# Optimization experiments

Hardware: AMD Instinct MI355X
Metric: run time of the kernel (lower is better)

The kernel has to match this reference:

```python
import jax, jax.numpy as jnp
import numpy as np

N, E, G, D, C = 50000, 800000, 512, 128, 10
BN_EPS = 1e-5

def setup_inputs() -> dict:
    key = jax.random.key(0)
    ks = jax.random.split(key, 12)
    inp = {
        'x': jnp.zeros((N,), dtype=jnp.int64 if jax.config.jax_enable_x64 else jnp.int32),
        'edge_index': jax.random.randint(ks[0], (2, E), 0, N),
        'batch_ids': jnp.sort(jax.random.randint(ks[1], (N,), 0, G)),
        'emb': jax.random.normal(ks[2], (1, D), jnp.float32),
        'W1a': jax.random.normal(ks[3], (D, D), jnp.float32) * 0.05,
        'b1a': jnp.zeros((D,), jnp.float32),
        'g1': jnp.ones((D,), jnp.float32),
        'be1': jnp.zeros((D,), jnp.float32),
        'W1b': jax.random.normal(ks[4], (D, D), jnp.float32) * 0.05,
        'b1b': jnp.zeros((D,), jnp.float32),
        'W2a': jax.random.normal(ks[5], (D, D), jnp.float32) * 0.05,
        'b2a': jnp.zeros((D,), jnp.float32),
        'g2': jnp.ones((D,), jnp.float32),
        'be2': jnp.zeros((D,), jnp.float32),
        'W2b': jax.random.normal(ks[6], (D, D), jnp.float32) * 0.05,
        'b2b': jnp.zeros((D,), jnp.float32),
        'Wm': jax.random.normal(ks[7], (D, C), jnp.float32) * 0.05,
        'bm': jnp.zeros((C,), jnp.float32),
        'Wx': jax.random.normal(ks[8], (D, C), jnp.float32) * 0.05,
        'bx': jnp.zeros((C,), jnp.float32),
        'ens_w': jnp.array([0.6, 0.4], jnp.float32),
    }
    return inp

def _gin_layer(h, src, dst, Wa, ba, g, be, Wb, bb):
    # GINConv, eps=0: mlp(x + sum_{j in N(i)} x_j)
    agg = jax.ops.segment_sum(h[src], dst, num_segments=N)  # [N, D]
    z = (h + agg) @ Wa + ba
    mu = jnp.mean(z, axis=0)
    var = jnp.var(z, axis=0)  # biased, as torch BN training forward
    z = (z - mu) * jax.lax.rsqrt(var + BN_EPS) * g + be
    z = jax.nn.relu(z)  # dropout is identity in eval
    return z @ Wb + bb

def reference(x, edge_index, batch_ids, emb, W1a, b1a, g1, be1, W1b, b1b,
              W2a, b2a, g2, be2, W2b, b2b, Wm, bm, Wx, bx, ens_w):
    src, dst = edge_index[0], edge_index[1]
    h0 = emb[x]  # [N, D] (all indices 0)
    h1 = _gin_layer(h0, src, dst, W1a, b1a, g1, be1, W1b, b1b)
    h2 = _gin_layer(h1, src, dst, W2a, b2a, g2, be2, W2b, b2b) + h1
    # global mean / max pooling over batch segments
    counts = jax.ops.segment_sum(jnp.ones((N,), h2.dtype), batch_ids, num_segments=G)
    mean_repr = jax.ops.segment_sum(h2, batch_ids, num_segments=G) / jnp.maximum(counts, 1.0)[:, None]
    max_repr = jax.ops.segment_max(h2, batch_ids, num_segments=G)
    max_repr = jnp.where(jnp.isfinite(max_repr), max_repr, 0.0)  # empty segments -> 0
    logits_mean = mean_repr @ Wm + bm
    logits_max = max_repr @ Wx + bx
    w = jax.nn.softmax(ens_w)
    ensemble_logits = w[0] * logits_mean + w[1] * logits_max
    return (ensemble_logits, logits_mean, logits_max, (mean_repr, max_repr))
```

## Files before the change

kernel.cpp:

```cpp
#include <hip/hip_runtime.h>
#include <math.h>

#define N_NODES  50000
#define N_EDGES  800000
#define N_GRAPHS 512
#define DIM      128
#define NCLS     10
#define KH       64
#define KW       32
#define KT       128
#define OVF_CAP  65536
#define BN_EPS   1e-5f

#define NB_GEMM  ((N_NODES + 63) / 64)


__global__ void k_zero(uint4* __restrict__ p, long long n4) {
    long long i = (long long)blockIdx.x * blockDim.x + threadIdx.x;
    if (i < n4) p[i] = make_uint4(0u, 0u, 0u, 0u);
}

__global__ void k_count_deg(const int* __restrict__ dst, int* __restrict__ deg) {
    int e = blockIdx.x * blockDim.x + threadIdx.x;
    if (e < N_EDGES) atomicAdd(&deg[dst[e]], 1);
}

__device__ inline int lower_bound_i(const int* __restrict__ a, int n, int v) {
    int lo = 0, hi = n;
    while (lo < hi) {
        int mid = (lo + hi) >> 1;
        if (a[mid] < v) lo = mid + 1; else hi = mid;
    }
    return lo;
}

__global__ __launch_bounds__(512) void k_prep2(
        const int* __restrict__ batch, int* __restrict__ seg,
        const int* __restrict__ deg,
        const float* __restrict__ emb, const float* __restrict__ W1a,
        const float* __restrict__ g1, const float* __restrict__ be1,
        float* __restrict__ A, float* __restrict__ B) {
    __shared__ unsigned long long sred[512];
    const int t = threadIdx.x;
    seg[t] = lower_bound_i(batch, N_NODES, t);
    if (t == 0) seg[N_GRAPHS] = N_NODES;
    unsigned long long s = 0;
    for (int i = t; i < N_NODES; i += 512) {
        unsigned long long d = (unsigned long long)(unsigned int)deg[i];
        s += d * d;
    }
    sred[t] = s;
    __syncthreads();
    for (int st = 256; st > 0; st >>= 1) {
        if (t < st) sred[t] += sred[t + st];
        __syncthreads();
    }
    if (t < DIM) {
        float u = 0.f;
        for (int k = 0; k < DIM; ++k) u += emb[k] * W1a[k * DIM + t];
        double mdeg = (double)N_EDGES / (double)N_NODES;
        double vdeg = (double)sred[0] / (double)N_NODES - mdeg * mdeg;
        float var = (float)((double)u * (double)u * vdeg);
        float rs  = rsqrtf(var + BN_EPS);
        float a   = u * rs * g1[t];
        A[t] = a;
        B[t] = be1[t] - (float)mdeg * a;
    }
}

__global__ void k_tables(const float* __restrict__ A, const float* __restrict__ B,
                         const float* __restrict__ W1b, const float* __restrict__ b1b,
                         const float* __restrict__ W2a,
                         float* __restrict__ table, float* __restrict__ table2) {
    int k = blockIdx.x, d = threadIdx.x;
    __shared__ float r[DIM];
    __shared__ float t[DIM];
    float kf = (float)k;
    r[d] = fmaxf(kf * A[d] + B[d], 0.f);
    __syncthreads();
    float acc = b1b[d];
    for (int j = 0; j < DIM; ++j) acc += r[j] * W1b[j * DIM + d];
    table[(size_t)k * DIM + d] = acc;
    t[d] = acc;
    __syncthreads();
    float acc2 = 0.f;
    for (int j = 0; j < DIM; ++j) acc2 += t[j] * W2a[j * DIM + d];
    table2[(size_t)k * DIM + d] = acc2;
}

__global__ void k_edges(const int* __restrict__ src, const int* __restrict__ dst,
                        const int* __restrict__ deg, unsigned int* __restrict__ m,
                        unsigned int* __restrict__ ovf_cnt, int* __restrict__ ovf_buf) {
    int e = blockIdx.x * blockDim.x + threadIdx.x;
    if (e >= N_EDGES) return;
    int s = src[e], dd = dst[e];
    int k = deg[s];
    if (k < KH) {
        atomicAdd(&m[(size_t)dd * KW + (k >> 1)], 1u << ((k & 1) << 4));
    } else {
        unsigned int idx = atomicAdd(ovf_cnt, 1u);
        if (idx < OVF_CAP) {
            ovf_buf[2 * idx] = dd;
            ovf_buf[2 * idx + 1] = k;
        }
    }
}

__global__ __launch_bounds__(256) void k_gemm1(
        const unsigned int* __restrict__ m, const int* __restrict__ deg,
        const float* __restrict__ table2, const float* __restrict__ b2a,
        float* __restrict__ z2, float* __restrict__ spart,
        const unsigned int* __restrict__ ovf_cnt, const int* __restrict__ ovf_buf) {
    __shared__ __align__(16) float lds_t2[64 * 128];
    __shared__ __align__(16) unsigned int lds_m[64 * 33];
    const int t = threadIdx.x;
    const int i0 = blockIdx.x * 64;
    #pragma unroll
    for (int q = 0; q < 8; ++q) {
        int idx = t + 256 * q;
        int row = idx >> 5, c = (idx & 31) << 2;
        *(float4*)&lds_t2[row * 128 + c] = *(const float4*)&table2[(size_t)row * 128 + c];
    }
    #pragma unroll
    for (int q = 0; q < 2; ++q) {
        int idx = t + 256 * q;
        int row = idx >> 3, c = (idx & 7) << 2;
        uint4 v = make_uint4(0u, 0u, 0u, 0u);
        if (i0 + row < N_NODES) v = *(const uint4*)&m[(size_t)(i0 + row) * KW + c];
        lds_m[row * 33 + c + 0] = v.x;
        lds_m[row * 33 + c + 1] = v.y;
        lds_m[row * 33 + c + 2] = v.z;
        lds_m[row * 33 + c + 3] = v.w;
    }
    __syncthreads();

    const int g = t >> 5;
    const int c4 = (t & 31) << 2;
    const int rbase = g * 8;
    float acc[8][4] = {};
    #pragma unroll 4
    for (int w = 0; w < KW; ++w) {
        float4 ta = *(const float4*)&lds_t2[(2 * w) * 128 + c4];
        float4 tb = *(const float4*)&lds_t2[(2 * w + 1) * 128 + c4];
        #pragma unroll
        for (int r = 0; r < 8; ++r) {
            unsigned int mw = lds_m[(rbase + r) * 33 + w];
            float lo = (float)(mw & 0xFFFFu);
            float hi = (float)(mw >> 16);
            acc[r][0] += lo * ta.x + hi * tb.x;
            acc[r][1] += lo * ta.y + hi * tb.y;
            acc[r][2] += lo * ta.z + hi * tb.z;
            acc[r][3] += lo * ta.w + hi * tb.w;
        }
    }

    unsigned int nov = *ovf_cnt;
    if (nov > OVF_CAP) nov = OVF_CAP;
    for (unsigned int u = 0; u < nov; ++u) {
        int dd = ovf_buf[2 * u];
        int r = dd - i0;
        if (r >= 0 && r < 64 && (r >> 3) == g) {
            int kk = ovf_buf[2 * u + 1]; if (kk > KT - 1) kk = KT - 1;
            float4 tv = *(const float4*)&table2[(size_t)kk * DIM + c4];
            acc[r & 7][0] += tv.x; acc[r & 7][1] += tv.y;
            acc[r & 7][2] += tv.z; acc[r & 7][3] += tv.w;
        }
    }

    float4 bb = *(const float4*)&b2a[c4];
    float s4[4] = {0.f, 0.f, 0.f, 0.f};
    float q4[4] = {0.f, 0.f, 0.f, 0.f};
    #pragma unroll
    for (int r = 0; r < 8; ++r) {
        int row = i0 + rbase + r;
        if (row < N_NODES) {
            int kk = deg[row];
            float4 self;
            if (kk < KH) self = *(const float4*)&lds_t2[kk * 128 + c4];
            else {
                if (kk > KT - 1) kk = KT - 1;
                self = *(const float4*)&table2[(size_t)kk * DIM + c4];
            }
            float v0 = acc[r][0] + self.x + bb.x;
            float v1 = acc[r][1] + self.y + bb.y;
            float v2 = acc[r][2] + self.z + bb.z;
            float v3 = acc[r][3] + self.w + bb.w;
            *(float4*)&z2[(size_t)row * DIM + c4] = make_float4(v0, v1, v2, v3);
            s4[0] += v0; q4[0] += v0 * v0;
            s4[1] += v1; q4[1] += v1 * v1;
            s4[2] += v2; q4[2] += v2 * v2;
            s4[3] += v3; q4[3] += v3 * v3;
        }
    }
    __syncthreads();
    float* red = (float*)lds_m;
    #pragma unroll
    for (int j = 0; j < 4; ++j) {
        red[g * 128 + c4 + j] = s4[j];
        red[1024 + g * 128 + c4 + j] = q4[j];
    }
    __syncthreads();
    if (t < 128) {
        float ss = 0.f, qq = 0.f;
        #pragma unroll
        for (int gg = 0; gg < 8; ++gg) {
            ss += red[gg * 128 + t];
            qq += red[1024 + gg * 128 + t];
        }
        spart[(size_t)blockIdx.x * 256 + t] = ss;
        spart[(size_t)blockIdx.x * 256 + 128 + t] = qq;
    }
}

__global__ __launch_bounds__(1024) void k_fin2(
        const float* __restrict__ spart,
        const float* __restrict__ g2, const float* __restrict__ be2,
        float* __restrict__ A2, float* __restrict__ B2) {
    __shared__ double red[4 * 256];
    int t = threadIdx.x & 255;
    int q = threadIdx.x >> 8;
    double acc = 0.0;
    #pragma unroll 4
    for (int b = q; b < NB_GEMM; b += 4) acc += (double)spart[(size_t)b * 256 + t];
    red[q * 256 + t] = acc;
    __syncthreads();
    if (threadIdx.x < 256)
        red[threadIdx.x] = red[threadIdx.x] + red[256 + threadIdx.x] +
                           red[512 + threadIdx.x] + red[768 + threadIdx.x];
    __syncthreads();
    if (threadIdx.x < 128) {
        double mu = red[threadIdx.x] / (double)N_NODES;
        double var = red[128 + threadIdx.x] / (double)N_NODES - mu * mu;
        float rs = rsqrtf((float)var + BN_EPS);
        float a = rs * g2[threadIdx.x];
        A2[threadIdx.x] = a;
        B2[threadIdx.x] = be2[threadIdx.x] - (float)mu * a;
    }
}

__global__ __launch_bounds__(256) void k_gemm2(
        const float* __restrict__ z2, const float* __restrict__ A2, const float* __restrict__ B2,
        const float* __restrict__ W2b, const float* __restrict__ b2b,
        const float* __restrict__ table, const int* __restrict__ deg,
        float* __restrict__ h2) {
    __shared__ __align__(16) float lds_zn[64 * 132];
    const int t = threadIdx.x;
    const int i0 = blockIdx.x * 64;
    #pragma unroll
    for (int q = 0; q < 8; ++q) {
        int idx = t + 256 * q;
        int row = idx >> 5, cc = (idx & 31) << 2;
        float4 zv = make_float4(0.f, 0.f, 0.f, 0.f);
        if (i0 + row < N_NODES) zv = *(const float4*)&z2[(size_t)(i0 + row) * DIM + cc];
        float4 av = *(const float4*)&A2[cc];
        float4 bv = *(const float4*)&B2[cc];
        lds_zn[row * 132 + cc + 0] = fmaxf(zv.x * av.x + bv.x, 0.f);
        lds_zn[row * 132 + cc + 1] = fmaxf(zv.y * av.y + bv.y, 0.f);
        lds_zn[row * 132 + cc + 2] = fmaxf(zv.z * av.z + bv.z, 0.f);
        lds_zn[row * 132 + cc + 3] = fmaxf(zv.w * av.w + bv.w, 0.f);
    }
    __syncthreads();

    const int g = t >> 5;
    const int c4 = (t & 31) << 2;
    const int rbase = g * 8;
    float acc[8][4] = {};
    #pragma unroll 2
    for (int kb = 0; kb < 32; ++kb) {
        const int k0 = kb * 4;
        float4 w0 = *(const float4*)&W2b[(size_t)(k0 + 0) * DIM + c4];
        float4 w1 = *(const float4*)&W2b[(size_t)(k0 + 1) * DIM + c4];
        float4 w2 = *(const float4*)&W2b[(size_t)(k0 + 2) * DIM + c4];
        float4 w3 = *(const float4*)&W2b[(size_t)(k0 + 3) * DIM + c4];
        #pragma unroll
        for (int r = 0; r < 8; ++r) {
            float4 zr = *(const float4*)&lds_zn[(rbase + r) * 132 + k0];
            acc[r][0] += zr.x * w0.x + zr.y * w1.x + zr.z * w2.x + zr.w * w3.x;
            acc[r][1] += zr.x * w0.y + zr.y * w1.y + zr.z * w2.y + zr.w * w3.y;
            acc[r][2] += zr.x * w0.z + zr.y * w1.z + zr.z * w2.z + zr.w * w3.z;
            acc[r][3] += zr.x * w0.w + zr.y * w1.w + zr.z * w2.w + zr.w * w3.w;
        }
    }

    float4 bbv = *(const float4*)&b2b[c4];
    #pragma unroll
    for (int r = 0; r < 8; ++r) {
        int row = i0 + rbase + r;
        if (row < N_NODES) {
            int kk = deg[row]; if (kk > KT - 1) kk = KT - 1;
            float4 tb = *(const float4*)&table[(size_t)kk * DIM + c4];
            float4 o;
            o.x = acc[r][0] + bbv.x + tb.x;
            o.y = acc[r][1] + bbv.y + tb.y;
            o.z = acc[r][2] + bbv.z + tb.z;
            o.w = acc[r][3] + bbv.w + tb.w;
            *(float4*)&h2[(size_t)row * DIM + c4] = o;
        }
    }
}

__global__ __launch_bounds__(1024) void k_poolhead(
        const float* __restrict__ h2, const int* __restrict__ seg,
        const float* __restrict__ Wm, const float* __restrict__ bm,
        const float* __restrict__ Wx, const float* __restrict__ bx,
        const float* __restrict__ ensw,
        float* __restrict__ out_ens, float* __restrict__ out_lm,
        float* __restrict__ out_lx,
        float* __restrict__ out_mean, float* __restrict__ out_max) {
    __shared__ float reds[32 * 132];
    __shared__ float redm[32 * 132];
    int g = blockIdx.x;
    int s0 = seg[g], e0 = seg[g + 1];
    int rg = threadIdx.x >> 5;
    int c4 = (threadIdx.x & 31) << 2;
    float s[4] = {0.f, 0.f, 0.f, 0.f};
    float mx[4] = {-INFINITY, -INFINITY, -INFINITY, -INFINITY};
    for (int i = s0 + rg; i < e0; i += 32) {
        float4 v = *(const float4*)&h2[(size_t)i * DIM + c4];
        s[0] += v.x; mx[0] = fmaxf(mx[0], v.x);
        s[1] += v.y; mx[1] = fmaxf(mx[1], v.y);
        s[2] += v.z; mx[2] = fmaxf(mx[2], v.z);
        s[3] += v.w; mx[3] = fmaxf(mx[3], v.w);
    }
    #pragma unroll
    for (int j = 0; j < 4; ++j) {
        reds[rg * 132 + c4 + j] = s[j];
        redm[rg * 132 + c4 + j] = mx[j];
    }
    __syncthreads();
    for (int step = 16; step >= 1; step >>= 1) {
        if (rg < step) {
            #pragma unroll
            for (int j = 0; j < 4; ++j) {
                reds[rg * 132 + c4 + j] += reds[(rg + step) * 132 + c4 + j];
                redm[rg * 132 + c4 + j] = fmaxf(redm[rg * 132 + c4 + j],
                                                redm[(rg + step) * 132 + c4 + j]);
            }
        }
        __syncthreads();
    }
    if (rg == 0) {
        int cnt = e0 - s0;
        float denom = (float)(cnt > 0 ? cnt : 1);
        #pragma unroll
        for (int j = 0; j < 4; ++j) {
            float mean = reds[c4 + j] / denom;
            float mxv  = (cnt > 0) ? redm[c4 + j] : 0.f;
            out_mean[(size_t)g * DIM + c4 + j] = mean;
            out_max[(size_t)g * DIM + c4 + j]  = mxv;
            reds[c4 + j] = mean;
            redm[c4 + j] = mxv;
        }
    }
    __syncthreads();
    int t = threadIdx.x;
    if (t < NCLS) {
        float lm = bm[t], lx = bx[t];
        for (int d = 0; d < DIM; ++d) {
            lm += reds[d] * Wm[d * NCLS + t];
            lx += redm[d] * Wx[d * NCLS + t];
        }
        float a0 = ensw[0], a1 = ensw[1];
        float mw = fmaxf(a0, a1);
        float e0v = expf(a0 - mw), e1v = expf(a1 - mw);
        float inv = 1.f / (e0v + e1v);
        out_lm[(size_t)g * NCLS + t] = lm;
        out_lx[(size_t)g * NCLS + t] = lx;
        out_ens[(size_t)g * NCLS + t] = (e0v * inv) * lm + (e1v * inv) * lx;
    }
}


extern "C" void kernel_launch(void* const* d_in, const int* in_sizes, int n_in,
                              void* d_out, int out_size, void* d_ws, size_t ws_size,
                              hipStream_t stream) {
    const int* edge = (const int*)d_in[1];
    const int* src = edge;
    const int* dst = edge + N_EDGES;
    const int* batch = (const int*)d_in[2];
    const float* emb = (const float*)d_in[3];
    const float* W1a = (const float*)d_in[4];
    const float* g1  = (const float*)d_in[6];
    const float* be1 = (const float*)d_in[7];
    const float* W1b = (const float*)d_in[8];
    const float* b1b = (const float*)d_in[9];
    const float* W2a = (const float*)d_in[10];
    const float* b2a = (const float*)d_in[11];
    const float* g2  = (const float*)d_in[12];
    const float* be2 = (const float*)d_in[13];
    const float* W2b = (const float*)d_in[14];
    const float* b2b = (const float*)d_in[15];
    const float* Wm  = (const float*)d_in[16];
    const float* bm  = (const float*)d_in[17];
    const float* Wx  = (const float*)d_in[18];
    const float* bx  = (const float*)d_in[19];
    const float* ensw = (const float*)d_in[20];

    char* ws = (char*)d_ws;
    size_t off = 0;
    auto take = [&](size_t bytes) {
        char* p = ws + off;
        off += (bytes + 511) & ~(size_t)511;
        return p;
    };
    int* deg                  = (int*)take((size_t)N_NODES * 4);
    unsigned int* m           = (unsigned int*)take((size_t)N_NODES * KW * 4);
    unsigned int* ovf_cnt     = (unsigned int*)take(4);
    size_t zbytes = off;
    float* spart              = (float*)take((size_t)NB_GEMM * 256 * 4);
    int* ovf_buf              = (int*)take((size_t)OVF_CAP * 2 * 4);
    float* table              = (float*)take((size_t)KT * DIM * 4);
    float* table2             = (float*)take((size_t)KT * DIM * 4);
    float* A                  = (float*)take(DIM * 4);
    float* B                  = (float*)take(DIM * 4);
    float* A2                 = (float*)take(DIM * 4);
    float* B2                 = (float*)take(DIM * 4);
    int* seg                  = (int*)take((size_t)(N_GRAPHS + 1) * 4);
    float* z2                 = (float*)take((size_t)N_NODES * DIM * 4);
    float* h2                 = (float*)take((size_t)N_NODES * DIM * 4);
    (void)ws_size; (void)in_sizes; (void)n_in; (void)out_size;

    float* out      = (float*)d_out;
    float* out_ens  = out;
    float* out_lm   = out + (size_t)N_GRAPHS * NCLS;
    float* out_lx   = out + 2 * (size_t)N_GRAPHS * NCLS;
    float* out_mean = out + 3 * (size_t)N_GRAPHS * NCLS;
    float* out_max  = out_mean + (size_t)N_GRAPHS * DIM;

    long long n4 = (long long)(zbytes >> 4);
    k_zero<<<(int)((n4 + 255) / 256), 256, 0, stream>>>((uint4*)ws, n4);
    k_count_deg<<<(N_EDGES + 255) / 256, 256, 0, stream>>>(dst, deg);
    k_edges<<<(N_EDGES + 255) / 256, 256, 0, stream>>>(src, dst, deg, m, ovf_cnt, ovf_buf);
    k_prep2<<<1, 512, 0, stream>>>(batch, seg, deg, emb, W1a, g1, be1, A, B);
    k_tables<<<KT, DIM, 0, stream>>>(A, B, W1b, b1b, W2a, table, table2);
    k_gemm1<<<NB_GEMM, 256, 0, stream>>>(m, deg, table2, b2a, z2, spart, ovf_cnt, ovf_buf);
    k_fin2<<<1, 1024, 0, stream>>>(spart, g2, be2, A2, B2);
    k_gemm2<<<NB_GEMM, 256, 0, stream>>>(z2, A2, B2, W2b, b2b, table, deg, h2);
    k_poolhead<<<N_GRAPHS, 1024, 0, stream>>>(h2, seg, Wm, bm, Wx, bx, ensw,
                                              out_ens, out_lm, out_lx, out_mean, out_max);
}
```

Baseline: 201.5 us.

## Recompute layer-2 pre-activations in gemm2 instead of storing z2; parallelize reductions

```diff
diff --git a/kernel.cpp b/kernel.cpp
--- a/kernel.cpp
+++ b/kernel.cpp
@@ -12,7 +12,10 @@
 #define OVF_CAP  65536
 #define BN_EPS   1e-5f
 
-#define NB_GEMM  ((N_NODES + 63) / 64)
+#define TR       32
+#define NB_GEMM  ((N_NODES + TR - 1) / TR)
+#define NB_DEG   32
+#define FIN_A    96
 
 
 __global__ void k_zero(uint4* __restrict__ p, long long n4) {
@@ -20,9 +23,15 @@
     if (i < n4) p[i] = make_uint4(0u, 0u, 0u, 0u);
 }
 
-__global__ void k_count_deg(const int* __restrict__ dst, int* __restrict__ deg) {
+__global__ void k_count_deg(const int4* __restrict__ dst4, int* __restrict__ deg) {
     int e = blockIdx.x * blockDim.x + threadIdx.x;
-    if (e < N_EDGES) atomicAdd(&deg[dst[e]], 1);
+    if (e < N_EDGES / 4) {
+        int4 d = dst4[e];
+        atomicAdd(&deg[d.x], 1);
+        atomicAdd(&deg[d.y], 1);
+        atomicAdd(&deg[d.z], 1);
+        atomicAdd(&deg[d.w], 1);
+    }
 }
 
 __device__ inline int lower_bound_i(const int* __restrict__ a, int n, int v) {
@@ -34,49 +43,51 @@
     return lo;
 }
 
-__global__ __launch_bounds__(512) void k_prep2(
-        const int* __restrict__ batch, int* __restrict__ seg,
-        const int* __restrict__ deg,
-        const float* __restrict__ emb, const float* __restrict__ W1a,
-        const float* __restrict__ g1, const float* __restrict__ be1,
-        float* __restrict__ A, float* __restrict__ B) {
-    __shared__ unsigned long long sred[512];
+__global__ __launch_bounds__(1024) void k_sumdeg2(
+        const int* __restrict__ deg, unsigned long long* __restrict__ dpart,
+        const int* __restrict__ batch, int* __restrict__ seg) {
+    __shared__ unsigned long long lds[1024];
     const int t = threadIdx.x;
-    seg[t] = lower_bound_i(batch, N_NODES, t);
-    if (t == 0) seg[N_GRAPHS] = N_NODES;
+    if (blockIdx.x == 0) {
+        if (t < N_GRAPHS) seg[t] = lower_bound_i(batch, N_NODES, t);
+        if (t == 0) seg[N_GRAPHS] = N_NODES;
+    }
     unsigned long long s = 0;
-    for (int i = t; i < N_NODES; i += 512) {
+    for (int i = blockIdx.x * 1024 + t; i < N_NODES; i += NB_DEG * 1024) {
         unsigned long long d = (unsigned long long)(unsigned int)deg[i];
         s += d * d;
     }
-    sred[t] = s;
-    __syncthreads();
-    for (int st = 256; st > 0; st >>= 1) {
-        if (t < st) sred[t] += sred[t + st];
+    lds[t] = s;
+    __syncthreads();
+    for (int st = 512; st > 0; st >>= 1) {
+        if (t < st) lds[t] += lds[t + st];
         __syncthreads();
     }
-    if (t < DIM) {
-        float u = 0.f;
-        for (int k = 0; k < DIM; ++k) u += emb[k] * W1a[k * DIM + t];
-        double mdeg = (double)N_EDGES / (double)N_NODES;
-        double vdeg = (double)sred[0] / (double)N_NODES - mdeg * mdeg;
-        float var = (float)((double)u * (double)u * vdeg);
-        float rs  = rsqrtf(var + BN_EPS);
-        float a   = u * rs * g1[t];
-        A[t] = a;
-        B[t] = be1[t] - (float)mdeg * a;
-    }
-}
-
-__global__ void k_tables(const float* __restrict__ A, const float* __restrict__ B,
+    if (t == 0) dpart[blockIdx.x] = lds[0];
+}
+
+__global__ void k_tables(const unsigned long long* __restrict__ dpart,
+                         const float* __restrict__ emb, const float* __restrict__ W1a,
+                         const float* __restrict__ g1, const float* __restrict__ be1,
                          const float* __restrict__ W1b, const float* __restrict__ b1b,
                          const float* __restrict__ W2a,
                          float* __restrict__ table, float* __restrict__ table2) {
     int k = blockIdx.x, d = threadIdx.x;
     __shared__ float r[DIM];
     __shared__ float t[DIM];
+    float u = 0.f;
+    for (int j = 0; j < DIM; ++j) u += emb[j] * W1a[j * DIM + d];
+    unsigned long long s2 = 0;
+    #pragma unroll 8
+    for (int b = 0; b < NB_DEG; ++b) s2 += dpart[b];
+    double mdeg = (double)N_EDGES / (double)N_NODES;
+    double vdeg = (double)s2 / (double)N_NODES - mdeg * mdeg;
+    float var = (float)((double)u * (double)u * vdeg);
+    float rs  = rsqrtf(var + BN_EPS);
+    float A   = u * rs * g1[d];
+    float B   = be1[d] - (float)mdeg * A;
     float kf = (float)k;
-    r[d] = fmaxf(kf * A[d] + B[d], 0.f);
+    r[d] = fmaxf(kf * A + B, 0.f);
     __syncthreads();
     float acc = b1b[d];
     for (int j = 0; j < DIM; ++j) acc += r[j] * W1b[j * DIM + d];
@@ -88,43 +99,41 @@
     table2[(size_t)k * DIM + d] = acc2;
 }
 
-__global__ void k_edges(const int* __restrict__ src, const int* __restrict__ dst,
+__global__ void k_edges(const int4* __restrict__ src4, const int4* __restrict__ dst4,
                         const int* __restrict__ deg, unsigned int* __restrict__ m,
                         unsigned int* __restrict__ ovf_cnt, int* __restrict__ ovf_buf) {
     int e = blockIdx.x * blockDim.x + threadIdx.x;
-    if (e >= N_EDGES) return;
-    int s = src[e], dd = dst[e];
-    int k = deg[s];
-    if (k < KH) {
-        atomicAdd(&m[(size_t)dd * KW + (k >> 1)], 1u << ((k & 1) << 4));
-    } else {
-        unsigned int idx = atomicAdd(ovf_cnt, 1u);
-        if (idx < OVF_CAP) {
-            ovf_buf[2 * idx] = dd;
-            ovf_buf[2 * idx + 1] = k;
-        }
-    }
-}
-
-__global__ __launch_bounds__(256) void k_gemm1(
+    if (e >= N_EDGES / 4) return;
+    int4 sv = src4[e];
+    int4 dv = dst4[e];
+    int ss[4] = {sv.x, sv.y, sv.z, sv.w};
+    int dd[4] = {dv.x, dv.y, dv.z, dv.w};
+    #pragma unroll
+    for (int j = 0; j < 4; ++j) {
+        int k = deg[ss[j]];
+        if (k < KH) {
+            atomicAdd(&m[(size_t)dd[j] * KW + (k >> 1)], 1u << ((k & 1) << 4));
+        } else {
+            unsigned int idx = atomicAdd(ovf_cnt, 1u);
+            if (idx < OVF_CAP) {
+                ovf_buf[2 * idx] = dd[j];
+                ovf_buf[2 * idx + 1] = k;
+            }
+        }
+    }
+}
+
+__global__ __launch_bounds__(256) void k_gemm1s(
         const unsigned int* __restrict__ m, const int* __restrict__ deg,
         const float* __restrict__ table2, const float* __restrict__ b2a,
-        float* __restrict__ z2, float* __restrict__ spart,
+        float* __restrict__ spart,
         const unsigned int* __restrict__ ovf_cnt, const int* __restrict__ ovf_buf) {
-    __shared__ __align__(16) float lds_t2[64 * 128];
-    __shared__ __align__(16) unsigned int lds_m[64 * 33];
+    __shared__ __align__(16) unsigned int lds_m[TR * 33];
+    __shared__ float red[2048];
     const int t = threadIdx.x;
-    const int i0 = blockIdx.x * 64;
-    #pragma unroll
-    for (int q = 0; q < 8; ++q) {
-        int idx = t + 256 * q;
-        int row = idx >> 5, c = (idx & 31) << 2;
-        *(float4*)&lds_t2[row * 128 + c] = *(const float4*)&table2[(size_t)row * 128 + c];
-    }
-    #pragma unroll
-    for (int q = 0; q < 2; ++q) {
-        int idx = t + 256 * q;
-        int row = idx >> 3, c = (idx & 7) << 2;
+    const int i0 = blockIdx.x * TR;
+    {
+        int row = t >> 3, c = (t & 7) << 2;
         uint4 v = make_uint4(0u, 0u, 0u, 0u);
         if (i0 + row < N_NODES) v = *(const uint4*)&m[(size_t)(i0 + row) * KW + c];
         lds_m[row * 33 + c + 0] = v.x;
@@ -136,14 +145,14 @@
 
     const int g = t >> 5;
     const int c4 = (t & 31) << 2;
-    const int rbase = g * 8;
-    float acc[8][4] = {};
+    const int rbase = g * 4;
+    float acc[4][4] = {};
     #pragma unroll 4
     for (int w = 0; w < KW; ++w) {
-        float4 ta = *(const float4*)&lds_t2[(2 * w) * 128 + c4];
-        float4 tb = *(const float4*)&lds_t2[(2 * w + 1) * 128 + c4];
+        float4 ta = *(const float4*)&table2[(size_t)(2 * w) * DIM + c4];
+        float4 tb = *(const float4*)&table2[(size_t)(2 * w + 1) * DIM + c4];
         #pragma unroll
-        for (int r = 0; r < 8; ++r) {
+        for (int r = 0; r < 4; ++r) {
             unsigned int mw = lds_m[(rbase + r) * 33 + w];
             float lo = (float)(mw & 0xFFFFu);
             float hi = (float)(mw >> 16);
@@ -153,17 +162,16 @@
             acc[r][3] += lo * ta.w + hi * tb.w;
         }
     }
-
     unsigned int nov = *ovf_cnt;
     if (nov > OVF_CAP) nov = OVF_CAP;
     for (unsigned int u = 0; u < nov; ++u) {
         int dd = ovf_buf[2 * u];
         int r = dd - i0;
-        if (r >= 0 && r < 64 && (r >> 3) == g) {
+        if (r >= 0 && r < TR && (r >> 2) == g) {
             int kk = ovf_buf[2 * u + 1]; if (kk > KT - 1) kk = KT - 1;
             float4 tv = *(const float4*)&table2[(size_t)kk * DIM + c4];
-            acc[r & 7][0] += tv.x; acc[r & 7][1] += tv.y;
-            acc[r & 7][2] += tv.z; acc[r & 7][3] += tv.w;
+            acc[r & 3][0] += tv.x; acc[r & 3][1] += tv.y;
+            acc[r & 3][2] += tv.z; acc[r & 3][3] += tv.w;
         }
     }
 
@@ -171,29 +179,21 @@
     float s4[4] = {0.f, 0.f, 0.f, 0.f};
     float q4[4] = {0.f, 0.f, 0.f, 0.f};
     #pragma unroll
-    for (int r = 0; r < 8; ++r) {
+    for (int r = 0; r < 4; ++r) {
         int row = i0 + rbase + r;
         if (row < N_NODES) {
-            int kk = deg[row];
-            float4 self;
-            if (kk < KH) self = *(const float4*)&lds_t2[kk * 128 + c4];
-            else {
-                if (kk > KT - 1) kk = KT - 1;
-                self = *(const float4*)&table2[(size_t)kk * DIM + c4];
-            }
+            int kk = deg[row]; if (kk > KT - 1) kk = KT - 1;
+            float4 self = *(const float4*)&table2[(size_t)kk * DIM + c4];
             float v0 = acc[r][0] + self.x + bb.x;
             float v1 = acc[r][1] + self.y + bb.y;
             float v2 = acc[r][2] + self.z + bb.z;
             float v3 = acc[r][3] + self.w + bb.w;
-            *(float4*)&z2[(size_t)row * DIM + c4] = make_float4(v0, v1, v2, v3);
             s4[0] += v0; q4[0] += v0 * v0;
             s4[1] += v1; q4[1] += v1 * v1;
             s4[2] += v2; q4[2] += v2 * v2;
             s4[3] += v3; q4[3] += v3 * v3;
         }
     }
-    __syncthreads();
-    float* red = (float*)lds_m;
     #pragma unroll
     for (int j = 0; j < 4; ++j) {
         red[g * 128 + c4 + j] = s4[j];
@@ -212,59 +212,116 @@
     }
 }
 
-__global__ __launch_bounds__(1024) void k_fin2(
-        const float* __restrict__ spart,
+__global__ __launch_bounds__(256) void k_fin2a(
+        const float* __restrict__ spart, double* __restrict__ spart2) {
+    const int t = threadIdx.x;
+    double s = 0.0;
+    for (int r = blockIdx.x; r < NB_GEMM; r += FIN_A)
+        s += (double)spart[(size_t)r * 256 + t];
+    spart2[(size_t)blockIdx.x * 256 + t] = s;
+}
+
+__global__ __launch_bounds__(256) void k_fin2b(
+        const double* __restrict__ spart2,
         const float* __restrict__ g2, const float* __restrict__ be2,
         float* __restrict__ A2, float* __restrict__ B2) {
-    __shared__ double red[4 * 256];
-    int t = threadIdx.x & 255;
-    int q = threadIdx.x >> 8;
-    double acc = 0.0;
-    #pragma unroll 4
-    for (int b = q; b < NB_GEMM; b += 4) acc += (double)spart[(size_t)b * 256 + t];
-    red[q * 256 + t] = acc;
-    __syncthreads();
-    if (threadIdx.x < 256)
-        red[threadIdx.x] = red[threadIdx.x] + red[256 + threadIdx.x] +
-                           red[512 + threadIdx.x] + red[768 + threadIdx.x];
-    __syncthreads();
-    if (threadIdx.x < 128) {
-        double mu = red[threadIdx.x] / (double)N_NODES;
-        double var = red[128 + threadIdx.x] / (double)N_NODES - mu * mu;
+    __shared__ double red[256];
+    const int t = threadIdx.x;
+    double s = 0.0;
+    #pragma unroll 8
+    for (int b = 0; b < FIN_A; ++b) s += spart2[(size_t)b * 256 + t];
+    red[t] = s;
+    __syncthreads();
+    if (t < 128) {
+        double mu = red[t] / (double)N_NODES;
+        double var = red[128 + t] / (double)N_NODES - mu * mu;
         float rs = rsqrtf((float)var + BN_EPS);
-        float a = rs * g2[threadIdx.x];
-        A2[threadIdx.x] = a;
-        B2[threadIdx.x] = be2[threadIdx.x] - (float)mu * a;
+        float a = rs * g2[t];
+        A2[t] = a;
+        B2[t] = be2[t] - (float)mu * a;
     }
 }
 
 __global__ __launch_bounds__(256) void k_gemm2(
-        const float* __restrict__ z2, const float* __restrict__ A2, const float* __restrict__ B2,
+        const unsigned int* __restrict__ m, const int* __restrict__ deg,
+        const float* __restrict__ table2, const float* __restrict__ b2a,
+        const float* __restrict__ A2, const float* __restrict__ B2,
         const float* __restrict__ W2b, const float* __restrict__ b2b,
-        const float* __restrict__ table, const int* __restrict__ deg,
-        float* __restrict__ h2) {
-    __shared__ __align__(16) float lds_zn[64 * 132];
+        const float* __restrict__ table, float* __restrict__ h2,
+        const unsigned int* __restrict__ ovf_cnt, const int* __restrict__ ovf_buf) {
+    __shared__ __align__(16) unsigned int lds_m[TR * 33];
+    __shared__ __align__(16) float lds_zn[TR * 132];
     const int t = threadIdx.x;
-    const int i0 = blockIdx.x * 64;
-    #pragma unroll
-    for (int q = 0; q < 8; ++q) {
-        int idx = t + 256 * q;
-        int row = idx >> 5, cc = (idx & 31) << 2;
-        float4 zv = make_float4(0.f, 0.f, 0.f, 0.f);
-        if (i0 + row < N_NODES) zv = *(const float4*)&z2[(size_t)(i0 + row) * DIM + cc];
-        float4 av = *(const float4*)&A2[cc];
-        float4 bv = *(const float4*)&B2[cc];
-        lds_zn[row * 132 + cc + 0] = fmaxf(zv.x * av.x + bv.x, 0.f);
-        lds_zn[row * 132 + cc + 1] = fmaxf(zv.y * av.y + bv.y, 0.f);
-        lds_zn[row * 132 + cc + 2] = fmaxf(zv.z * av.z + bv.z, 0.f);
-        lds_zn[row * 132 + cc + 3] = fmaxf(zv.w * av.w + bv.w, 0.f);
+    const int i0 = blockIdx.x * TR;
+    {
+        int row = t >> 3, c = (t & 7) << 2;
+        uint4 v = make_uint4(0u, 0u, 0u, 0u);
+        if (i0 + row < N_NODES) v = *(const uint4*)&m[(size_t)(i0 + row) * KW + c];
+        lds_m[row * 33 + c + 0] = v.x;
+        lds_m[row * 33 + c + 1] = v.y;
+        lds_m[row * 33 + c + 2] = v.z;
+        lds_m[row * 33 + c + 3] = v.w;
     }
     __syncthreads();
 
     const int g = t >> 5;
     const int c4 = (t & 31) << 2;
-    const int rbase = g * 8;
-    float acc[8][4] = {};
+    const int rbase = g * 4;
+    float acc[4][4] = {};
+    #pragma unroll 4
+    for (int w = 0; w < KW; ++w) {
+        float4 ta = *(const float4*)&table2[(size_t)(2 * w) * DIM + c4];
+        float4 tb = *(const float4*)&table2[(size_t)(2 * w + 1) * DIM + c4];
+        #pragma unroll
+        for (int r = 0; r < 4; ++r) {
+            unsigned int mw = lds_m[(rbase + r) * 33 + w];
+            float lo = (float)(mw & 0xFFFFu);
+            float hi = (float)(mw >> 16);
+            acc[r][0] += lo * ta.x + hi * tb.x;
+            acc[r][1] += lo * ta.y + hi * tb.y;
+            acc[r][2] += lo * ta.z + hi * tb.z;
+            acc[r][3] += lo * ta.w + hi * tb.w;
+        }
+    }
+    unsigned int nov = *ovf_cnt;
+    if (nov > OVF_CAP) nov = OVF_CAP;
+    for (unsigned int u = 0; u < nov; ++u) {
+        int dd = ovf_buf[2 * u];
+        int r = dd - i0;
+        if (r >= 0 && r < TR && (r >> 2) == g) {
+            int kk = ovf_buf[2 * u + 1]; if (kk > KT - 1) kk = KT - 1;
+            float4 tv = *(const float4*)&table2[(size_t)kk * DIM + c4];
+            acc[r & 3][0] += tv.x; acc[r & 3][1] += tv.y;
+            acc[r & 3][2] += tv.z; acc[r & 3][3] += tv.w;
+        }
+    }
+
+    float4 bb = *(const float4*)&b2a[c4];
+    float4 av = *(const float4*)&A2[c4];
+    float4 bv = *(const float4*)&B2[c4];
+    int kks[4];
+    #pragma unroll
+    for (int r = 0; r < 4; ++r) {
+        int row = i0 + rbase + r;
+        float z0 = 0.f, z1 = 0.f, z2v = 0.f, z3 = 0.f;
+        kks[r] = 0;
+        if (row < N_NODES) {
+            int kk = deg[row]; if (kk > KT - 1) kk = KT - 1;
+            kks[r] = kk;
+            float4 self = *(const float4*)&table2[(size_t)kk * DIM + c4];
+            z0 = fmaxf((acc[r][0] + self.x + bb.x) * av.x + bv.x, 0.f);
+            z1 = fmaxf((acc[r][1] + self.y + bb.y) * av.y + bv.y, 0.f);
+            z2v = fmaxf((acc[r][2] + self.z + bb.z) * av.z + bv.z, 0.f);
+            z3 = fmaxf((acc[r][3] + self.w + bb.w) * av.w + bv.w, 0.f);
+        }
+        lds_zn[(rbase + r) * 132 + c4 + 0] = z0;
+        lds_zn[(rbase + r) * 132 + c4 + 1] = z1;
+        lds_zn[(rbase + r) * 132 + c4 + 2] = z2v;
+        lds_zn[(rbase + r) * 132 + c4 + 3] = z3;
+    }
+    __syncthreads();
+
+    float acc2[4][4] = {};
     #pragma unroll 2
     for (int kb = 0; kb < 32; ++kb) {
         const int k0 = kb * 4;
@@ -273,27 +330,26 @@
         float4 w2 = *(const float4*)&W2b[(size_t)(k0 + 2) * DIM + c4];
         float4 w3 = *(const float4*)&W2b[(size_t)(k0 + 3) * DIM + c4];
         #pragma unroll
-        for (int r = 0; r < 8; ++r) {
+        for (int r = 0; r < 4; ++r) {
             float4 zr = *(const float4*)&lds_zn[(rbase + r) * 132 + k0];
-            acc[r][0] += zr.x * w0.x + zr.y * w1.x + zr.z * w2.x + zr.w * w3.x;
-            acc[r][1] += zr.x * w0.y + zr.y * w1.y + zr.z * w2.y + zr.w * w3.y;
-            acc[r][2] += zr.x * w0.z + zr.y * w1.z + zr.z * w2.z + zr.w * w3.z;
-            acc[r][3] += zr.x * w0.w + zr.y * w1.w + zr.z * w2.w + zr.w * w3.w;
+            acc2[r][0] += zr.x * w0.x + zr.y * w1.x + zr.z * w2.x + zr.w * w3.x;
+            acc2[r][1] += zr.x * w0.y + zr.y * w1.y + zr.z * w2.y + zr.w * w3.y;
+            acc2[r][2] += zr.x * w0.z + zr.y * w1.z + zr.z * w2.z + zr.w * w3.z;
+            acc2[r][3] += zr.x * w0.w + zr.y * w1.w + zr.z * w2.w + zr.w * w3.w;
         }
     }
 
     float4 bbv = *(const float4*)&b2b[c4];
     #pragma unroll
-    for (int r = 0; r < 8; ++r) {
+    for (int r = 0; r < 4; ++r) {
         int row = i0 + rbase + r;
         if (row < N_NODES) {
-            int kk = deg[row]; if (kk > KT - 1) kk = KT - 1;
-            float4 tb = *(const float4*)&table[(size_t)kk * DIM + c4];
+            float4 tb = *(const float4*)&table[(size_t)kks[r] * DIM + c4];
             float4 o;
-            o.x = acc[r][0] + bbv.x + tb.x;
-            o.y = acc[r][1] + bbv.y + tb.y;
-            o.z = acc[r][2] + bbv.z + tb.z;
-            o.w = acc[r][3] + bbv.w + tb.w;
+            o.x = acc2[r][0] + bbv.x + tb.x;
+            o.y = acc2[r][1] + bbv.y + tb.y;
+            o.z = acc2[r][2] + bbv.z + tb.z;
+            o.w = acc2[r][3] + bbv.w + tb.w;
             *(float4*)&h2[(size_t)row * DIM + c4] = o;
         }
     }
@@ -407,16 +463,15 @@
     unsigned int* m           = (unsigned int*)take((size_t)N_NODES * KW * 4);
     unsigned int* ovf_cnt     = (unsigned int*)take(4);
     size_t zbytes = off;
+    unsigned long long* dpart = (unsigned long long*)take((size_t)NB_DEG * 8);
     float* spart              = (float*)take((size_t)NB_GEMM * 256 * 4);
+    double* spart2            = (double*)take((size_t)FIN_A * 256 * 8);
     int* ovf_buf              = (int*)take((size_t)OVF_CAP * 2 * 4);
     float* table              = (float*)take((size_t)KT * DIM * 4);
     float* table2             = (float*)take((size_t)KT * DIM * 4);
-    float* A                  = (float*)take(DIM * 4);
-    float* B                  = (float*)take(DIM * 4);
     float* A2                 = (float*)take(DIM * 4);
     float* B2                 = (float*)take(DIM * 4);
     int* seg                  = (int*)take((size_t)(N_GRAPHS + 1) * 4);
-    float* z2                 = (float*)take((size_t)N_NODES * DIM * 4);
     float* h2                 = (float*)take((size_t)N_NODES * DIM * 4);
     (void)ws_size; (void)in_sizes; (void)n_in; (void)out_size;
 
@@ -429,13 +484,17 @@
 
     long long n4 = (long long)(zbytes >> 4);
     k_zero<<<(int)((n4 + 255) / 256), 256, 0, stream>>>((uint4*)ws, n4);
-    k_count_deg<<<(N_EDGES + 255) / 256, 256, 0, stream>>>(dst, deg);
-    k_edges<<<(N_EDGES + 255) / 256, 256, 0, stream>>>(src, dst, deg, m, ovf_cnt, ovf_buf);
-    k_prep2<<<1, 512, 0, stream>>>(batch, seg, deg, emb, W1a, g1, be1, A, B);
-    k_tables<<<KT, DIM, 0, stream>>>(A, B, W1b, b1b, W2a, table, table2);
-    k_gemm1<<<NB_GEMM, 256, 0, stream>>>(m, deg, table2, b2a, z2, spart, ovf_cnt, ovf_buf);
-    k_fin2<<<1, 1024, 0, stream>>>(spart, g2, be2, A2, B2);
-    k_gemm2<<<NB_GEMM, 256, 0, stream>>>(z2, A2, B2, W2b, b2b, table, deg, h2);
+    k_count_deg<<<(N_EDGES / 4 + 255) / 256, 256, 0, stream>>>((const int4*)dst, deg);
+    k_sumdeg2<<<NB_DEG, 1024, 0, stream>>>(deg, dpart, batch, seg);
+    k_tables<<<KT, DIM, 0, stream>>>(dpart, emb, W1a, g1, be1, W1b, b1b, W2a,
+                                     table, table2);
+    k_edges<<<(N_EDGES / 4 + 255) / 256, 256, 0, stream>>>(
+        (const int4*)src, (const int4*)dst, deg, m, ovf_cnt, ovf_buf);
+    k_gemm1s<<<NB_GEMM, 256, 0, stream>>>(m, deg, table2, b2a, spart, ovf_cnt, ovf_buf);
+    k_fin2a<<<FIN_A, 256, 0, stream>>>(spart, spart2);
+    k_fin2b<<<1, 256, 0, stream>>>(spart2, g2, be2, A2, B2);
+    k_gemm2<<<NB_GEMM, 256, 0, stream>>>(m, deg, table2, b2a, A2, B2, W2b, b2b,
+                                         table, h2, ovf_cnt, ovf_buf);
     k_poolhead<<<N_GRAPHS, 1024, 0, stream>>>(h2, seg, Wm, bm, Wx, bx, ensw,
                                               out_ens, out_lm, out_lx, out_mean, out_max);
 }
```

Measured after the change: 196.6 us. -2.4%, faster.
